# Optimization experiments

Measured on AMD Instinct MI355X. Metric: run time of the kernel, lower is better.

## Reference

```python
import jax, jax.numpy as jnp
import numpy as np

B, S, H, A, E = 64, 1024, 1024, 512, 512


def setup_inputs() -> dict:
    key = jax.random.key(0)
    ks = jax.random.split(key, 13)
    sc = 0.02
    return {
        "inputs": jax.random.normal(ks[0], (B, E), jnp.float32),
        "states": jax.random.normal(ks[1], (B, H), jnp.float32),
        "encoded": jax.random.normal(ks[2], (B, S, H), jnp.float32),
        "W_enc": jax.random.normal(ks[3], (H, A), jnp.float32) * sc,
        "b_enc": jax.random.normal(ks[4], (A,), jnp.float32) * sc,
        "W_dec": jax.random.normal(ks[5], (H, A), jnp.float32) * sc,
        "b_dec": jax.random.normal(ks[6], (A,), jnp.float32) * sc,
        "w_out": jax.random.normal(ks[7], (A,), jnp.float32) * sc,
        "b_out": jax.random.normal(ks[8], (1,), jnp.float32) * sc,
        "W_ih": jax.random.normal(ks[9], (E + H, 3 * H), jnp.float32) * sc,
        "b_ih": jax.random.normal(ks[10], (3 * H,), jnp.float32) * sc,
        "W_hh": jax.random.normal(ks[11], (H, 3 * H), jnp.float32) * sc,
        "b_hh": jax.random.normal(ks[12], (3 * H,), jnp.float32) * sc,
    }


def reference(inputs, states, encoded, W_enc, b_enc, W_dec, b_dec, w_out, b_out,
              W_ih, b_ih, W_hh, b_hh):
    # setup_memory: project encoder states once  [B,S,H] @ [H,A] -> [B,S,A]
    enc_proj = jnp.einsum('bsh,ha->bsa', encoded, W_enc) + b_enc
    # Bahdanau additive attention
    dec_proj = states @ W_dec + b_dec                       # [B,A]
    scores = jnp.einsum('bsa,a->bs', jnp.tanh(enc_proj + dec_proj[:, None, :]), w_out) + b_out[0]
    weights = jax.nn.softmax(scores, axis=1)                # [B,S]
    attention = jnp.einsum('bs,bsh->bh', weights, encoded)  # [B,H]
    x = jnp.concatenate([inputs, attention], axis=-1)       # [B,E+H]
    # GRUCell (PyTorch gate order r, z, n)
    gi = x @ W_ih + b_ih                                    # [B,3H]
    gh = states @ W_hh + b_hh                               # [B,3H]
    i_r, i_z, i_n = jnp.split(gi, 3, axis=-1)
    h_r, h_z, h_n = jnp.split(gh, 3, axis=-1)
    r = jax.nn.sigmoid(i_r + h_r)
    z = jax.nn.sigmoid(i_z + h_z)
    n = jnp.tanh(i_n + r * h_n)
    h_new = (1.0 - z) * n + z * states
    return h_new
```

## Files before the change

### kernel.cpp

```cpp
#include <hip/hip_runtime.h>
#include <hip/hip_bf16.h>


typedef __attribute__((ext_vector_type(8))) __bf16 bf16x8;
typedef __attribute__((ext_vector_type(4))) __bf16 bf16x4;
typedef __attribute__((ext_vector_type(4))) float f32x4;

__device__ __forceinline__ float fast_tanh(float x) {
  float xa = fminf(fmaxf(x, -15.f), 15.f);
  float e = __expf(2.f * xa);
  return (e - 1.f) / (e + 1.f);
}

#define GLOAD16(G, L)                                                              \
  __builtin_amdgcn_global_load_lds(                                                \
      (const __attribute__((address_space(1))) unsigned int*)(const void*)(G),     \
      (__attribute__((address_space(3))) unsigned int*)(void*)(L), 16, 0, 0)

__global__ __launch_bounds__(256) void conv_kernel(const float* __restrict__ in,
                                                   __bf16* __restrict__ out, long n16) {
  long stride = (long)gridDim.x * 256;
  for (long i = (long)blockIdx.x * 256 + threadIdx.x; i < n16; i += stride) {
    const f32x4* p = (const f32x4*)(in + i * 16);
    f32x4 v0 = p[0], v1 = p[1], v2 = p[2], v3 = p[3];
    bf16x8 o0, o1;
#pragma unroll
    for (int j = 0; j < 4; ++j) {
      o0[j] = (__bf16)v0[j]; o0[4 + j] = (__bf16)v1[j];
      o1[j] = (__bf16)v2[j]; o1[4 + j] = (__bf16)v3[j];
    }
    *(bf16x8*)(out + i * 16) = o0;
    *(bf16x8*)(out + i * 16 + 8) = o1;
  }
}

__global__ __launch_bounds__(256) void wenc_t_kernel(const float* __restrict__ W,
                                                     __bf16* __restrict__ Wt) {
  __shared__ float tile[32][33];
  int k0 = blockIdx.x * 32, a0 = blockIdx.y * 32;
  int tid = threadIdx.x;
  int r = tid >> 3, c4 = (tid & 7) * 4;
  f32x4 v = *(const f32x4*)(W + (long)(k0 + r) * 512 + a0 + c4);
  tile[r][c4 + 0] = v.x; tile[r][c4 + 1] = v.y;
  tile[r][c4 + 2] = v.z; tile[r][c4 + 3] = v.w;
  __syncthreads();
  int a = tid >> 3, k4 = (tid & 7) * 4;
  bf16x4 o = { (__bf16)tile[k4 + 0][a], (__bf16)tile[k4 + 1][a],
               (__bf16)tile[k4 + 2][a], (__bf16)tile[k4 + 3][a] };
  *(bf16x4*)(Wt + (long)(a0 + a) * 1024 + k0 + k4) = o;
}

__global__ __launch_bounds__(256) void dec_proj_kernel(
    const float* __restrict__ states, const float* __restrict__ W_dec,
    const float* __restrict__ b_enc, const float* __restrict__ b_dec,
    float* __restrict__ addv) {
  int b = blockIdx.x, tid = threadIdx.x;
  int a = blockIdx.y * 256 + tid;
  __shared__ float sl[1024];
  for (int i = tid; i < 1024; i += 256) sl[i] = states[b * 1024 + i];
  __syncthreads();
  float c0 = 0.f, c1 = 0.f, c2 = 0.f, c3 = 0.f;
#pragma unroll 4
  for (int i = 0; i < 256; ++i) {
    c0 += sl[i]         * W_dec[(i)        * 512 + a];
    c1 += sl[i + 256]   * W_dec[(i + 256)  * 512 + a];
    c2 += sl[i + 512]   * W_dec[(i + 512)  * 512 + a];
    c3 += sl[i + 768]   * W_dec[(i + 768)  * 512 + a];
  }
  addv[b * 512 + a] = c0 + c1 + c2 + c3 + b_enc[a] + b_dec[a];
}

__global__ __launch_bounds__(512, 2) void enc_score_kernel(
    const __bf16* __restrict__ encB,
    const __bf16* __restrict__ Wt,
    const float* __restrict__ addv,
    const float* __restrict__ w_out,
    float* __restrict__ psc)
{
  __shared__ __attribute__((aligned(16))) char smem[135168];
  float* red = (float*)(smem + 131072);

  const int d = blockIdx.x;
  const int xcd = d & 7;
  const int slot = d >> 3;
  const int bn = slot & 1;
  const int bm = ((slot >> 1) << 3) | xcd;

  const int tid = threadIdx.x;
  const int lane = tid & 63;
  const int wid = tid >> 6;
  const int wr = wid >> 2;
  const int wc = wid & 3;
  const int lr = lane & 15;
  const int lkb = lane >> 4;

  const long row0 = (long)bm * 256;
  const int col0 = bn * 256;

  const int sk8 = (tid & 3) ^ ((tid >> 3) & 3);
  const __bf16* gA = encB + (row0 + (tid >> 2)) * 1024 + sk8 * 8;
  const __bf16* gB = Wt + (long)(col0 + (tid >> 2)) * 1024 + sk8 * 8;
  const int ldsW = wid * 1024;

  const int foff = (lkb ^ ((lr >> 1) & 3)) << 4;
  const int aRowB = (wr * 128 + lr) * 64;
  const int bColB = (wc * 64 + lr) * 64;

  f32x4 acc[8][4];
#pragma unroll
  for (int m = 0; m < 8; ++m)
#pragma unroll
    for (int n = 0; n < 4; ++n) acc[m][n] = (f32x4){0.f, 0.f, 0.f, 0.f};

#define STAGE(SBUF, KT) do {                                                       \
    const __bf16* _a = gA + (KT) * 32;                                             \
    const __bf16* _b = gB + (KT) * 32;                                             \
    char* _base = smem + (SBUF) * 32768;                                           \
    GLOAD16(_a,          _base + ldsW);                                            \
    GLOAD16(_a + 131072, _base + 8192 + ldsW);                                     \
    GLOAD16(_b,          _base + 16384 + ldsW);                                    \
    GLOAD16(_b + 131072, _base + 24576 + ldsW);                                    \
  } while (0)

#define COMPUTE(COFF) do {                                                         \
    const char* _Ab = smem + (COFF);                                               \
    const char* _Bb = _Ab + 16384;                                                 \
    bf16x8 _af[8], _bv[4];                                                         \
    _Pragma("unroll") for (int _m = 0; _m < 8; ++_m)                               \
      _af[_m] = *(const bf16x8*)(_Ab + aRowB + _m * 1024 + foff);                  \
    _Pragma("unroll") for (int _n = 0; _n < 4; ++_n)                               \
      _bv[_n] = *(const bf16x8*)(_Bb + bColB + _n * 1024 + foff);                  \
    __builtin_amdgcn_s_setprio(1);                                                 \
    _Pragma("unroll") for (int _m = 0; _m < 8; ++_m)                               \
      _Pragma("unroll") for (int _n = 0; _n < 4; ++_n)                             \
        acc[_m][_n] =                                                              \
            __builtin_amdgcn_mfma_f32_16x16x32_bf16(_af[_m], _bv[_n], acc[_m][_n], 0, 0, 0); \
    __builtin_amdgcn_s_setprio(0);                                                 \
  } while (0)

#define WAITBAR(N) do {                                                            \
    asm volatile("s_waitcnt vmcnt(" #N ")" ::: "memory");                          \
    __builtin_amdgcn_sched_barrier(0);                                             \
    __builtin_amdgcn_s_barrier();                                                  \
    __builtin_amdgcn_sched_barrier(0);                                             \
  } while (0)

  STAGE(0, 0);
  STAGE(1, 1);
  STAGE(2, 2);

  for (int kt = 0; kt < 29; ++kt) {
    WAITBAR(8);
    STAGE((kt + 3) & 3, kt + 3);
    __builtin_amdgcn_sched_barrier(0);
    COMPUTE((kt & 3) * 32768);
  }
  WAITBAR(8);
  COMPUTE(1 * 32768);
  WAITBAR(4);
  COMPUTE(2 * 32768);
  WAITBAR(0);
  COMPUTE(3 * 32768);

#undef STAGE
#undef COMPUTE
#undef WAITBAR

  const int b = bm >> 2;
  const float* addvb = addv + b * 512;
  float rowsum[8][4];
#pragma unroll
  for (int m = 0; m < 8; ++m)
#pragma unroll
    for (int reg = 0; reg < 4; ++reg) rowsum[m][reg] = 0.f;

#pragma unroll
  for (int m = 0; m < 8; ++m) {
#pragma unroll
    for (int n = 0; n < 4; ++n) {
      int col = col0 + wc * 64 + n * 16 + lr;
      float av = addvb[col];
      float wo = w_out[col];
#pragma unroll
      for (int reg = 0; reg < 4; ++reg)
        rowsum[m][reg] += fast_tanh(acc[m][n][reg] + av) * wo;
    }
  }
#pragma unroll
  for (int m = 0; m < 8; ++m)
#pragma unroll
    for (int reg = 0; reg < 4; ++reg) {
      float v = rowsum[m][reg];
      v += __shfl_xor(v, 1, 64);
      v += __shfl_xor(v, 2, 64);
      v += __shfl_xor(v, 4, 64);
      v += __shfl_xor(v, 8, 64);
      rowsum[m][reg] = v;
    }
  __syncthreads();
  if (lr == 0) {
#pragma unroll
    for (int m = 0; m < 8; ++m)
#pragma unroll
      for (int reg = 0; reg < 4; ++reg)
        red[(wr * 128 + m * 16 + lkb * 4 + reg) * 4 + wc] = rowsum[m][reg];
  }
  __syncthreads();
  if (tid < 256)
    psc[(long)bn * 65536 + row0 + tid] =
        red[tid * 4] + red[tid * 4 + 1] + red[tid * 4 + 2] + red[tid * 4 + 3];
}

__global__ __launch_bounds__(256) void softmax_kernel(const float* __restrict__ psc,
                                                      float* __restrict__ wts) {
  int b = blockIdx.x, tid = threadIdx.x;
  __shared__ float sred[8];
  float sc[4];
  float mx = -1e30f;
#pragma unroll
  for (int i = 0; i < 4; ++i) {
    long r = (long)b * 1024 + tid + i * 256;
    sc[i] = psc[r] + psc[65536 + r];
    mx = fmaxf(mx, sc[i]);
  }
  for (int off = 1; off < 64; off <<= 1) mx = fmaxf(mx, __shfl_xor(mx, off, 64));
  if ((tid & 63) == 0) sred[tid >> 6] = mx;
  __syncthreads();
  mx = fmaxf(fmaxf(sred[0], sred[1]), fmaxf(sred[2], sred[3]));
  float e[4], sum = 0.f;
#pragma unroll
  for (int i = 0; i < 4; ++i) {
    e[i] = __expf(sc[i] - mx);
    sum += e[i];
  }
  for (int off = 1; off < 64; off <<= 1) sum += __shfl_xor(sum, off, 64);
  if ((tid & 63) == 0) sred[4 + (tid >> 6)] = sum;
  __syncthreads();
  sum = sred[4] + sred[5] + sred[6] + sred[7];
  float inv = 1.f / sum;
#pragma unroll
  for (int i = 0; i < 4; ++i) wts[(long)b * 1024 + tid + i * 256] = e[i] * inv;
}

__global__ __launch_bounds__(128) void att_part_bf16_kernel(const __bf16* __restrict__ encB,
                                                            const float* __restrict__ wts,
                                                            float* __restrict__ attp) {
  int chunk = blockIdx.x;
  int b = blockIdx.y;
  int tid = threadIdx.x;
  const __bf16* base = encB + ((long)b * 1024 + chunk * 64) * 1024 + tid * 8;
  const float* w = wts + b * 1024 + chunk * 64;
  float a0[8], a1[8];
#pragma unroll
  for (int j = 0; j < 8; ++j) { a0[j] = 0.f; a1[j] = 0.f; }
#pragma unroll 4
  for (int s = 0; s < 64; s += 2) {
    bf16x8 v0 = *(const bf16x8*)(base + (long)s * 1024);
    bf16x8 v1 = *(const bf16x8*)(base + (long)(s + 1) * 1024);
    float w0 = w[s], w1 = w[s + 1];
#pragma unroll
    for (int j = 0; j < 8; ++j) {
      a0[j] += (float)v0[j] * w0;
      a1[j] += (float)v1[j] * w1;
    }
  }
  float* o = attp + ((long)(b * 16 + chunk)) * 1024 + tid * 8;
#pragma unroll
  for (int j = 0; j < 8; ++j) o[j] = a0[j] + a1[j];
}

__global__ __launch_bounds__(256) void xcat_kernel(const float* __restrict__ inputs,
                                                   const float* __restrict__ attp,
                                                   float* __restrict__ xcat) {
  int b = blockIdx.y;
  int k = blockIdx.x * 256 + threadIdx.x;
  float v;
  if (k < 512) {
    v = inputs[b * 512 + k];
  } else {
    int h = k - 512;
    v = 0.f;
#pragma unroll
    for (int c = 0; c < 16; ++c) v += attp[((long)(b * 16 + c)) * 1024 + h];
  }
  xcat[(long)b * 1536 + k] = v;
}

__global__ __launch_bounds__(512) void gru_gemv_kernel(
    const float* __restrict__ xcat, const float* __restrict__ states,
    const float* __restrict__ W_ih, const float* __restrict__ b_ih,
    const float* __restrict__ W_hh, const float* __restrict__ b_hh,
    float* __restrict__ gi, float* __restrict__ gh) {
  __shared__ float sx[12288];
  const int dd = blockIdx.x;
  const int xcd = dd & 7;
  const int n = dd >> 3;
  const int cgrp = xcd + 8 * (n >> 3);
  const int bg = n & 7;
  const int tid = threadIdx.x;
  const int lcol = tid & 255;
  const int bsel = (tid >> 8) * 4;

  if (cgrp < 12) {
    const int col = cgrp * 256 + lcol;
    const float* xb = xcat + (long)bg * 8 * 1536;
    for (int i = tid; i < 3072; i += 512) ((f32x4*)sx)[i] = ((const f32x4*)xb)[i];
    __syncthreads();
    float a0 = b_ih[col], a1 = a0, a2 = a0, a3 = a0;
    const float* x0 = sx + (bsel + 0) * 1536;
    const float* x1 = sx + (bsel + 1) * 1536;
    const float* x2 = sx + (bsel + 2) * 1536;
    const float* x3 = sx + (bsel + 3) * 1536;
    for (int k = 0; k < 1536; k += 4) {
      f32x4 v0 = *(const f32x4*)(x0 + k);
      f32x4 v1 = *(const f32x4*)(x1 + k);
      f32x4 v2 = *(const f32x4*)(x2 + k);
      f32x4 v3 = *(const f32x4*)(x3 + k);
#pragma unroll
      for (int j = 0; j < 4; ++j) {
        float w = W_ih[(long)(k + j) * 3072 + col];
        a0 += v0[j] * w; a1 += v1[j] * w; a2 += v2[j] * w; a3 += v3[j] * w;
      }
    }
    long o = (long)(bg * 8 + bsel) * 3072 + col;
    gi[o] = a0; gi[o + 3072] = a1; gi[o + 6144] = a2; gi[o + 9216] = a3;
  } else {
    const int col = (cgrp - 12) * 256 + lcol;
    const float* sb = states + (long)bg * 8 * 1024;
    for (int i = tid; i < 2048; i += 512) ((f32x4*)sx)[i] = ((const f32x4*)sb)[i];
    __syncthreads();
    float a0 = b_hh[col], a1 = a0, a2 = a0, a3 = a0;
    const float* x0 = sx + (bsel + 0) * 1024;
    const float* x1 = sx + (bsel + 1) * 1024;
    const float* x2 = sx + (bsel + 2) * 1024;
    const float* x3 = sx + (bsel + 3) * 1024;
    for (int k = 0; k < 1024; k += 4) {
      f32x4 v0 = *(const f32x4*)(x0 + k);
      f32x4 v1 = *(const f32x4*)(x1 + k);
      f32x4 v2 = *(const f32x4*)(x2 + k);
      f32x4 v3 = *(const f32x4*)(x3 + k);
#pragma unroll
      for (int j = 0; j < 4; ++j) {
        float w = W_hh[(long)(k + j) * 3072 + col];
        a0 += v0[j] * w; a1 += v1[j] * w; a2 += v2[j] * w; a3 += v3[j] * w;
      }
    }
    long o = (long)(bg * 8 + bsel) * 3072 + col;
    gh[o] = a0; gh[o + 3072] = a1; gh[o + 6144] = a2; gh[o + 9216] = a3;
  }
}

__global__ __launch_bounds__(256) void gate_kernel(const float* __restrict__ gi,
                                                   const float* __restrict__ gh,
                                                   const float* __restrict__ states,
                                                   float* __restrict__ out) {
  int b = blockIdx.y;
  int j = blockIdx.x * 256 + threadIdx.x;
  long o = (long)b * 3072;
  float ir = gi[o + j], hr = gh[o + j];
  float iz = gi[o + 1024 + j], hz = gh[o + 1024 + j];
  float in_ = gi[o + 2048 + j], hn = gh[o + 2048 + j];
  float r = 1.f / (1.f + __expf(-(ir + hr)));
  float z = 1.f / (1.f + __expf(-(iz + hz)));
  float n = fast_tanh(in_ + r * hn);
  out[(long)b * 1024 + j] = (1.f - z) * n + z * states[(long)b * 1024 + j];
}

extern "C" void kernel_launch(void* const* d_in, const int* in_sizes, int n_in,
                              void* d_out, int out_size, void* d_ws, size_t ws_size,
                              hipStream_t stream) {
  const float* inputs  = (const float*)d_in[0];
  const float* states  = (const float*)d_in[1];
  const float* encoded = (const float*)d_in[2];
  const float* W_enc   = (const float*)d_in[3];
  const float* b_enc   = (const float*)d_in[4];
  const float* W_dec   = (const float*)d_in[5];
  const float* b_dec   = (const float*)d_in[6];
  const float* w_out   = (const float*)d_in[7];
  const float* W_ih    = (const float*)d_in[9];
  const float* b_ih    = (const float*)d_in[10];
  const float* W_hh    = (const float*)d_in[11];
  const float* b_hh    = (const float*)d_in[12];
  float* out = (float*)d_out;
  float* ws = (float*)d_ws;

  const long ENC_ELEMS = 64L * 1024 * 1024;
  const long ENCB_FLOATS = ENC_ELEMS / 2;

  __bf16* encB = (__bf16*)ws;
  float* base = ws + ENCB_FLOATS;

  float* addv = base;
  float* psc  = base + 32768;
  float* wts  = base + 163840;
  float* attp = base + 229376;
  float* xcat = base + 1277952;
  float* gi   = base + 1376256;
  float* gh   = base + 1572864;
  __bf16* Wt  = (__bf16*)(base + 1769472);

  conv_kernel<<<4096, 256, 0, stream>>>(encoded, encB, ENC_ELEMS / 16);

  wenc_t_kernel<<<dim3(32, 16), 256, 0, stream>>>(W_enc, Wt);

  dim3 gA(64, 2);
  dec_proj_kernel<<<gA, 256, 0, stream>>>(states, W_dec, b_enc, b_dec, addv);

  enc_score_kernel<<<512, 512, 0, stream>>>(encB, Wt, addv, w_out, psc);

  softmax_kernel<<<64, 256, 0, stream>>>(psc, wts);

  dim3 gD(16, 64);
  att_part_bf16_kernel<<<gD, 128, 0, stream>>>(encB, wts, attp);

  dim3 gE(6, 64);
  xcat_kernel<<<gE, 256, 0, stream>>>(inputs, attp, xcat);

  gru_gemv_kernel<<<192, 512, 0, stream>>>(xcat, states, W_ih, b_ih, W_hh, b_hh, gi, gh);

  dim3 gG(4, 64);
  gate_kernel<<<gG, 256, 0, stream>>>(gi, gh, states, out);
}
```

Before: 337.2 us.

## Shrink score GEMM tile to 256x128 with 3-stage pipeline and split attention rows

The encoder-score GEMM tile shrinks from 256x256 to 256x128, the LDS ring drops from four stages to three, and the launch doubles to 1024 blocks with four column partials reduced in softmax. Together with the smaller accumulator this lets more blocks stay resident per CU for better latency hiding, at the cost of reading the A operand twice as often. The attention-weighted-sum kernel now uses 256 threads, with two row interleaves combined through shared memory, to raise memory-level parallelism. Workspace offsets are moved to fit the larger partial-score buffer.

```diff
diff --git a/kernel.cpp b/kernel.cpp
--- a/kernel.cpp
+++ b/kernel.cpp
@@ -70,32 +70,32 @@
   addv[b * 512 + a] = c0 + c1 + c2 + c3 + b_enc[a] + b_dec[a];
 }
 
-__global__ __launch_bounds__(512, 2) void enc_score_kernel(
+__global__ __launch_bounds__(512, 4) void enc_score_kernel(
     const __bf16* __restrict__ encB,
     const __bf16* __restrict__ Wt,
     const float* __restrict__ addv,
     const float* __restrict__ w_out,
     float* __restrict__ psc)
 {
-  __shared__ __attribute__((aligned(16))) char smem[135168];
-  float* red = (float*)(smem + 131072);
+  __shared__ __attribute__((aligned(16))) char smem[75776];
+  float* red = (float*)(smem + 73728);
 
   const int d = blockIdx.x;
   const int xcd = d & 7;
   const int slot = d >> 3;
-  const int bn = slot & 1;
-  const int bm = ((slot >> 1) << 3) | xcd;
+  const int bn = slot & 3;
+  const int bm = ((slot >> 2) << 3) | xcd;
 
   const int tid = threadIdx.x;
   const int lane = tid & 63;
   const int wid = tid >> 6;
-  const int wr = wid >> 2;
-  const int wc = wid & 3;
+  const int wr = wid >> 1;
+  const int wc = wid & 1;
   const int lr = lane & 15;
   const int lkb = lane >> 4;
 
   const long row0 = (long)bm * 256;
-  const int col0 = bn * 256;
+  const int col0 = bn * 128;
 
   const int sk8 = (tid & 3) ^ ((tid >> 3) & 3);
   const __bf16* gA = encB + (row0 + (tid >> 2)) * 1024 + sk8 * 8;
@@ -103,35 +103,34 @@
   const int ldsW = wid * 1024;
 
   const int foff = (lkb ^ ((lr >> 1) & 3)) << 4;
-  const int aRowB = (wr * 128 + lr) * 64;
+  const int aRowB = (wr * 64 + lr) * 64;
   const int bColB = (wc * 64 + lr) * 64;
 
-  f32x4 acc[8][4];
-#pragma unroll
-  for (int m = 0; m < 8; ++m)
+  f32x4 acc[4][4];
+#pragma unroll
+  for (int m = 0; m < 4; ++m)
 #pragma unroll
     for (int n = 0; n < 4; ++n) acc[m][n] = (f32x4){0.f, 0.f, 0.f, 0.f};
 
 #define STAGE(SBUF, KT) do {                                                       \
     const __bf16* _a = gA + (KT) * 32;                                             \
     const __bf16* _b = gB + (KT) * 32;                                             \
-    char* _base = smem + (SBUF) * 32768;                                           \
+    char* _base = smem + (SBUF) * 24576;                                           \
     GLOAD16(_a,          _base + ldsW);                                            \
     GLOAD16(_a + 131072, _base + 8192 + ldsW);                                     \
     GLOAD16(_b,          _base + 16384 + ldsW);                                    \
-    GLOAD16(_b + 131072, _base + 24576 + ldsW);                                    \
   } while (0)
 
-#define COMPUTE(COFF) do {                                                         \
-    const char* _Ab = smem + (COFF);                                               \
+#define COMPUTE(CBUF) do {                                                         \
+    const char* _Ab = smem + (CBUF) * 24576;                                       \
     const char* _Bb = _Ab + 16384;                                                 \
-    bf16x8 _af[8], _bv[4];                                                         \
-    _Pragma("unroll") for (int _m = 0; _m < 8; ++_m)                               \
+    bf16x8 _af[4], _bv[4];                                                         \
+    _Pragma("unroll") for (int _m = 0; _m < 4; ++_m)                               \
       _af[_m] = *(const bf16x8*)(_Ab + aRowB + _m * 1024 + foff);                  \
     _Pragma("unroll") for (int _n = 0; _n < 4; ++_n)                               \
       _bv[_n] = *(const bf16x8*)(_Bb + bColB + _n * 1024 + foff);                  \
     __builtin_amdgcn_s_setprio(1);                                                 \
-    _Pragma("unroll") for (int _m = 0; _m < 8; ++_m)                               \
+    _Pragma("unroll") for (int _m = 0; _m < 4; ++_m)                               \
       _Pragma("unroll") for (int _n = 0; _n < 4; ++_n)                             \
         acc[_m][_n] =                                                              \
             __builtin_amdgcn_mfma_f32_16x16x32_bf16(_af[_m], _bv[_n], acc[_m][_n], 0, 0, 0); \
@@ -145,37 +144,41 @@
     __builtin_amdgcn_sched_barrier(0);                                             \
   } while (0)
 
+#define ITER(KT, CBUF, SBUF) do {                                                  \
+    WAITBAR(3);                             \
+    STAGE(SBUF, (KT) + 2);               \
+    __builtin_amdgcn_sched_barrier(0);                                             \
+    COMPUTE(CBUF);                                                                 \
+  } while (0)
+
   STAGE(0, 0);
   STAGE(1, 1);
-  STAGE(2, 2);
-
-  for (int kt = 0; kt < 29; ++kt) {
-    WAITBAR(8);
-    STAGE((kt + 3) & 3, kt + 3);
-    __builtin_amdgcn_sched_barrier(0);
-    COMPUTE((kt & 3) * 32768);
-  }
-  WAITBAR(8);
-  COMPUTE(1 * 32768);
-  WAITBAR(4);
-  COMPUTE(2 * 32768);
+
+  for (int k3 = 0; k3 < 30; k3 += 3) {
+    ITER(k3 + 0, 0, 2);
+    ITER(k3 + 1, 1, 0);
+    ITER(k3 + 2, 2, 1);
+  }
+  WAITBAR(3);
+  COMPUTE(0);
   WAITBAR(0);
-  COMPUTE(3 * 32768);
+  COMPUTE(1);
 
 #undef STAGE
 #undef COMPUTE
 #undef WAITBAR
+#undef ITER
 
   const int b = bm >> 2;
   const float* addvb = addv + b * 512;
-  float rowsum[8][4];
-#pragma unroll
-  for (int m = 0; m < 8; ++m)
+  float rowsum[4][4];
+#pragma unroll
+  for (int m = 0; m < 4; ++m)
 #pragma unroll
     for (int reg = 0; reg < 4; ++reg) rowsum[m][reg] = 0.f;
 
 #pragma unroll
-  for (int m = 0; m < 8; ++m) {
+  for (int m = 0; m < 4; ++m) {
 #pragma unroll
     for (int n = 0; n < 4; ++n) {
       int col = col0 + wc * 64 + n * 16 + lr;
@@ -187,7 +190,7 @@
     }
   }
 #pragma unroll
-  for (int m = 0; m < 8; ++m)
+  for (int m = 0; m < 4; ++m)
 #pragma unroll
     for (int reg = 0; reg < 4; ++reg) {
       float v = rowsum[m][reg];
@@ -200,15 +203,14 @@
   __syncthreads();
   if (lr == 0) {
 #pragma unroll
-    for (int m = 0; m < 8; ++m)
+    for (int m = 0; m < 4; ++m)
 #pragma unroll
       for (int reg = 0; reg < 4; ++reg)
-        red[(wr * 128 + m * 16 + lkb * 4 + reg) * 4 + wc] = rowsum[m][reg];
+        red[(wr * 64 + m * 16 + lkb * 4 + reg) * 2 + wc] = rowsum[m][reg];
   }
   __syncthreads();
   if (tid < 256)
-    psc[(long)bn * 65536 + row0 + tid] =
-        red[tid * 4] + red[tid * 4 + 1] + red[tid * 4 + 2] + red[tid * 4 + 3];
+    psc[(long)bn * 65536 + row0 + tid] = red[tid * 2] + red[tid * 2 + 1];
 }
 
 __global__ __launch_bounds__(256) void softmax_kernel(const float* __restrict__ psc,
@@ -220,7 +222,7 @@
 #pragma unroll
   for (int i = 0; i < 4; ++i) {
     long r = (long)b * 1024 + tid + i * 256;
-    sc[i] = psc[r] + psc[65536 + r];
+    sc[i] = psc[r] + psc[65536 + r] + psc[2 * 65536 + r] + psc[3 * 65536 + r];
     mx = fmaxf(mx, sc[i]);
   }
   for (int off = 1; off < 64; off <<= 1) mx = fmaxf(mx, __shfl_xor(mx, off, 64));
@@ -242,31 +244,41 @@
   for (int i = 0; i < 4; ++i) wts[(long)b * 1024 + tid + i * 256] = e[i] * inv;
 }
 
-__global__ __launch_bounds__(128) void att_part_bf16_kernel(const __bf16* __restrict__ encB,
+__global__ __launch_bounds__(256) void att_part_bf16_kernel(const __bf16* __restrict__ encB,
                                                             const float* __restrict__ wts,
                                                             float* __restrict__ attp) {
   int chunk = blockIdx.x;
   int b = blockIdx.y;
   int tid = threadIdx.x;
-  const __bf16* base = encB + ((long)b * 1024 + chunk * 64) * 1024 + tid * 8;
-  const float* w = wts + b * 1024 + chunk * 64;
+  int h8 = tid & 127;
+  int sh = tid >> 7;
+  __shared__ float sacc[1024];
+  const __bf16* base = encB + ((long)b * 1024 + chunk * 64 + sh) * 1024 + h8 * 8;
+  const float* w = wts + b * 1024 + chunk * 64 + sh;
   float a0[8], a1[8];
 #pragma unroll
   for (int j = 0; j < 8; ++j) { a0[j] = 0.f; a1[j] = 0.f; }
 #pragma unroll 4
-  for (int s = 0; s < 64; s += 2) {
+  for (int s = 0; s < 64; s += 4) {
     bf16x8 v0 = *(const bf16x8*)(base + (long)s * 1024);
-    bf16x8 v1 = *(const bf16x8*)(base + (long)(s + 1) * 1024);
-    float w0 = w[s], w1 = w[s + 1];
+    bf16x8 v1 = *(const bf16x8*)(base + (long)(s + 2) * 1024);
+    float w0 = w[s], w1 = w[s + 2];
 #pragma unroll
     for (int j = 0; j < 8; ++j) {
       a0[j] += (float)v0[j] * w0;
       a1[j] += (float)v1[j] * w1;
     }
   }
-  float* o = attp + ((long)(b * 16 + chunk)) * 1024 + tid * 8;
-#pragma unroll
-  for (int j = 0; j < 8; ++j) o[j] = a0[j] + a1[j];
+  if (sh) {
+#pragma unroll
+    for (int j = 0; j < 8; ++j) sacc[h8 * 8 + j] = a0[j] + a1[j];
+  }
+  __syncthreads();
+  if (!sh) {
+    float* o = attp + ((long)(b * 16 + chunk)) * 1024 + h8 * 8;
+#pragma unroll
+    for (int j = 0; j < 8; ++j) o[j] = a0[j] + a1[j] + sacc[h8 * 8 + j];
+  }
 }
 
 __global__ __launch_bounds__(256) void xcat_kernel(const float* __restrict__ inputs,
@@ -392,12 +404,12 @@
 
   float* addv = base;
   float* psc  = base + 32768;
-  float* wts  = base + 163840;
-  float* attp = base + 229376;
-  float* xcat = base + 1277952;
-  float* gi   = base + 1376256;
-  float* gh   = base + 1572864;
-  __bf16* Wt  = (__bf16*)(base + 1769472);
+  float* wts  = base + 294912;
+  float* attp = base + 360448;
+  float* xcat = base + 1409024;
+  float* gi   = base + 1507328;
+  float* gh   = base + 1703936;
+  __bf16* Wt  = (__bf16*)(base + 1900544);
 
   conv_kernel<<<4096, 256, 0, stream>>>(encoded, encB, ENC_ELEMS / 16);
 
@@ -406,12 +418,12 @@
   dim3 gA(64, 2);
   dec_proj_kernel<<<gA, 256, 0, stream>>>(states, W_dec, b_enc, b_dec, addv);
 
-  enc_score_kernel<<<512, 512, 0, stream>>>(encB, Wt, addv, w_out, psc);
+  enc_score_kernel<<<1024, 512, 0, stream>>>(encB, Wt, addv, w_out, psc);
 
   softmax_kernel<<<64, 256, 0, stream>>>(psc, wts);
 
   dim3 gD(16, 64);
-  att_part_bf16_kernel<<<gD, 128, 0, stream>>>(encB, wts, attp);
+  att_part_bf16_kernel<<<gD, 256, 0, stream>>>(encB, wts, attp);
 
   dim3 gE(6, 64);
   xcat_kernel<<<gE, 256, 0, stream>>>(inputs, attp, xcat);
```

Result: no change. 340.4 us (+0.9%).
